# Kernel tuning notes

Hardware: AMD Instinct MI355X
Metric: run time of the kernel (lower is better)

Reference implementation:

```python
import jax, jax.numpy as jnp
import numpy as np

N_NODES = 50000
N_EDGES = 800000
D = 64
NUM_GRAPHS = 64


def setup_inputs() -> dict:
    key = jax.random.key(0)
    ks = jax.random.split(key, 8)
    node_features = jax.random.normal(ks[0], (N_NODES, D), dtype=jnp.float32)
    edge_index = jax.random.randint(ks[1], (2, N_EDGES), 0, N_NODES, dtype=jnp.int32)
    edge_weight = jax.random.uniform(ks[2], (N_EDGES,), dtype=jnp.float32)
    batch = jnp.sort(jax.random.randint(ks[3], (N_NODES,), 0, NUM_GRAPHS, dtype=jnp.int32))
    scale = 1.0 / np.sqrt(D)
    W1 = jax.random.normal(ks[4], (D, D), dtype=jnp.float32) * scale
    b1 = jnp.zeros((D,), dtype=jnp.float32)
    W2 = jax.random.normal(ks[5], (D, D), dtype=jnp.float32) * scale
    b2 = jnp.zeros((D,), dtype=jnp.float32)
    return {"node_features": node_features, "edge_index": edge_index,
            "edge_weight": edge_weight, "batch": batch,
            "W1": W1, "b1": b1, "W2": W2, "b2": b2}


def gcn_conv(x, row, col, ew, W, b, n_nodes):
    # PyG GCNConv: add self-loops (weight 1), symmetric normalization,
    # x' = norm-weighted scatter of (x @ W) over edges, plus bias.
    loop = jnp.arange(n_nodes, dtype=row.dtype)
    r = jnp.concatenate([row, loop])
    c = jnp.concatenate([col, loop])
    w = jnp.concatenate([ew, jnp.ones((n_nodes,), dtype=ew.dtype)])
    deg = jax.ops.segment_sum(w, c, num_segments=n_nodes)  # [N]
    dis = jnp.where(deg > 0, jax.lax.rsqrt(deg), 0.0)
    norm = dis[r] * w * dis[c]                             # [E+N]
    xw = x @ W                                             # [N, D_out]
    msg = xw[r] * norm[:, None]                            # gather + scale
    out = jax.ops.segment_sum(msg, c, num_segments=n_nodes)
    return out + b


def reference(node_features, edge_index, edge_weight, batch, W1, b1, W2, b2):
    row, col = edge_index[0], edge_index[1]
    x = node_features.astype(jnp.float32)
    # conv layers (all but final pooling layer) each followed by ReLU
    x = jax.nn.relu(gcn_conv(x, row, col, edge_weight, W1, b1, N_NODES))
    x = jax.nn.relu(gcn_conv(x, row, col, edge_weight, W2, b2, N_NODES))
    # MeanAggregation pooling over graph ids
    sums = jax.ops.segment_sum(x, batch, num_segments=NUM_GRAPHS)       # [G, D]
    cnts = jax.ops.segment_sum(jnp.ones((x.shape[0],), x.dtype), batch,
                               num_segments=NUM_GRAPHS)                 # [G]
    return sums / jnp.maximum(cnts, 1.0)[:, None]
```

## Files before the change

### kernel.cpp

```cpp
#include <hip/hip_runtime.h>
#include <hip/hip_fp16.h>

#define NN 50000
#define NE 800000
#define DD 64
#define NG 64

#define NBKT 196
#define MAXB 5120
#define SRTB 7168
#define P1CH 2048
#define P1NB ((NE + P1CH - 1) / P1CH)

__global__ __launch_bounds__(256) void bin_k(const int* __restrict__ ei,
                                             const float* __restrict__ ew,
                                             int* __restrict__ bucket_cnt,
                                             unsigned int* __restrict__ tmp_pay,
                                             unsigned char* __restrict__ tmp_c8) {
    __shared__ int hist[NBKT];
    __shared__ int basec[NBKT];
    const int t = threadIdx.x;
    const int e0 = blockIdx.x * P1CH;
    for (int i = t; i < NBKT; i += 256) hist[i] = 0;
    __syncthreads();
    int rr[8]; int cc[8]; float wwf[8];
    #pragma unroll
    for (int i = 0; i < 8; ++i) {
        int e = e0 + i * 256 + t;
        if (e < NE) {
            rr[i] = ei[e]; cc[i] = ei[NE + e]; wwf[i] = ew[e];
            atomicAdd(&hist[cc[i] >> 8], 1);
        } else cc[i] = -1;
    }
    __syncthreads();
    for (int i = t; i < NBKT; i += 256)
        basec[i] = (hist[i] > 0) ? (i * MAXB + atomicAdd(&bucket_cnt[i], hist[i])) : 0;
    __syncthreads();
    #pragma unroll
    for (int i = 0; i < 8; ++i) {
        if (cc[i] >= 0) {
            int b = cc[i] >> 8;
            int slot = atomicAdd(&basec[b], 1);
            unsigned int hb = (unsigned int)__half_as_ushort(__float2half(wwf[i]));
            tmp_pay[slot] = (hb << 16) | (unsigned int)rr[i];
            tmp_c8[slot] = (unsigned char)(cc[i] & 255);
        }
    }
}

__global__ __launch_bounds__(256) void build_k(const int* __restrict__ bucket_cnt,
                                               const unsigned int* __restrict__ tmp_pay,
                                               const unsigned char* __restrict__ tmp_c8,
                                               unsigned int* __restrict__ srt,
                                               int2* __restrict__ rowse,
                                               float* __restrict__ dis) {
    __shared__ int hist[256];
    __shared__ int cursor[256];
    __shared__ float degf[256];
    __shared__ int wtot[4];
    const int b = blockIdx.x;
    const int t = threadIdx.x;
    const int cntb = bucket_cnt[b];
    const int tbase = b * MAXB;
    hist[t] = 0; degf[t] = 0.0f;
    __syncthreads();
    for (int i = t; i < cntb; i += 256) atomicAdd(&hist[tmp_c8[tbase + i]], 1);
    __syncthreads();
    const int v = hist[t];
    const int pv = (v + 7) & ~7;
    int pre = pv;
    #pragma unroll
    for (int off = 1; off < 64; off <<= 1) {
        int u = __shfl_up(pre, off);
        if ((t & 63) >= off) pre += u;
    }
    if ((t & 63) == 63) wtot[t >> 6] = pre;
    __syncthreads();
    int woff = 0;
    for (int i = 0; i < (t >> 6); ++i) woff += wtot[i];
    const int start = b * SRTB + woff + pre - pv;
    cursor[t] = start;
    __syncthreads();
    for (int i = t; i < cntb; i += 256) {
        unsigned int u = tmp_pay[tbase + i];
        int c8 = tmp_c8[tbase + i];
        int slot = atomicAdd(&cursor[c8], 1);
        srt[slot] = u;
        float w = __half2float(__ushort_as_half((unsigned short)(u >> 16)));
        atomicAdd(&degf[c8], w);
    }
    __syncthreads();
    for (int i = start + v; i < start + pv; ++i) srt[i] = 0u;
    const int node = b * 256 + t;
    if (node < NN) {
        rowse[node] = make_int2(start, pv);
        dis[node] = rsqrtf(1.0f + degf[t]);
    }
}

template<bool ACT>
__global__ __launch_bounds__(256, 4) void gemm_k(
    const float* __restrict__ X, const float* __restrict__ W,
    const float* __restrict__ bias_prev, const float* __restrict__ dis,
    __half* __restrict__ Ah)
{
    __shared__ float Ws[64][64];
    __shared__ float Xs[64][68];
    const int t = threadIdx.x;
    const int row0 = blockIdx.x * 64;

    #pragma unroll
    for (int s = t; s < 64 * 64; s += 256) ((float*)Ws)[s] = W[s];
    #pragma unroll
    for (int s = t; s < 64 * 64; s += 256) {
        int r = s >> 6, k = s & 63;
        int row = row0 + r;
        if (row >= NN) row = NN - 1;
        float v = X[(size_t)row * DD + k];
        if (ACT) v = fmaxf(v + bias_prev[k], 0.0f);
        Xs[r][k] = v;
    }
    __syncthreads();

    const int tc = t & 15;
    const int tr = t >> 4;
    float4 acc[4];
    #pragma unroll
    for (int i = 0; i < 4; ++i) acc[i] = make_float4(0.f, 0.f, 0.f, 0.f);

    #pragma unroll 2
    for (int kc = 0; kc < 16; ++kc) {
        const int k = kc * 4;
        float4 w0 = *reinterpret_cast<const float4*>(&Ws[k + 0][tc * 4]);
        float4 w1 = *reinterpret_cast<const float4*>(&Ws[k + 1][tc * 4]);
        float4 w2 = *reinterpret_cast<const float4*>(&Ws[k + 2][tc * 4]);
        float4 w3 = *reinterpret_cast<const float4*>(&Ws[k + 3][tc * 4]);
        #pragma unroll
        for (int i = 0; i < 4; ++i) {
            float4 xv = *reinterpret_cast<const float4*>(&Xs[tr * 4 + i][k]);
            acc[i].x += xv.x * w0.x + xv.y * w1.x + xv.z * w2.x + xv.w * w3.x;
            acc[i].y += xv.x * w0.y + xv.y * w1.y + xv.z * w2.y + xv.w * w3.y;
            acc[i].z += xv.x * w0.z + xv.y * w1.z + xv.z * w2.z + xv.w * w3.z;
            acc[i].w += xv.x * w0.w + xv.y * w1.w + xv.z * w2.w + xv.w * w3.w;
        }
    }

    #pragma unroll
    for (int i = 0; i < 4; ++i) {
        int row = row0 + tr * 4 + i;
        if (row >= NN) break;
        float d = dis[row];
        __half2 h0 = __floats2half2_rn(acc[i].x * d, acc[i].y * d);
        __half2 h1 = __floats2half2_rn(acc[i].z * d, acc[i].w * d);
        uint2 st;
        st.x = *reinterpret_cast<unsigned int*>(&h0);
        st.y = *reinterpret_cast<unsigned int*>(&h1);
        *reinterpret_cast<uint2*>(&Ah[(size_t)row * DD + tc * 4]) = st;
    }
}

__global__ __launch_bounds__(256) void gather_k(
    const int2* __restrict__ rowse, const unsigned int* __restrict__ srt,
    const float* __restrict__ dis,
    const __half2* __restrict__ Ah2, float* __restrict__ B)
{
    const int node = blockIdx.x * 4 + (threadIdx.x >> 6);
    const int wl = threadIdx.x & 63;
    const int h = wl >> 5;
    const int l = wl & 31;
    if (node >= NN) return;
    const int2 se = rowse[node];
    float ax0 = 0.f, ay0 = 0.f, ax1 = 0.f, ay1 = 0.f;
    if (h == 0) {
        __half2 s = Ah2[(size_t)node * 32 + l];
        ax0 = __half2float(__low2half(s));
        ay0 = __half2float(__high2half(s));
    }
    const unsigned int* p = srt + se.x + h * 4;
    for (int n = se.y; n > 0; n -= 8, p += 8) {
        uint4 u = *reinterpret_cast<const uint4*>(p);
        __half2 a0 = Ah2[(size_t)(u.x & 0xffffu) * 32 + l];
        __half2 a1 = Ah2[(size_t)(u.y & 0xffffu) * 32 + l];
        __half2 a2 = Ah2[(size_t)(u.z & 0xffffu) * 32 + l];
        __half2 a3 = Ah2[(size_t)(u.w & 0xffffu) * 32 + l];
        float w0 = __half2float(__ushort_as_half((unsigned short)(u.x >> 16)));
        float w1 = __half2float(__ushort_as_half((unsigned short)(u.y >> 16)));
        float w2 = __half2float(__ushort_as_half((unsigned short)(u.z >> 16)));
        float w3 = __half2float(__ushort_as_half((unsigned short)(u.w >> 16)));
        ax0 += w0 * __half2float(__low2half(a0));
        ay0 += w0 * __half2float(__high2half(a0));
        ax1 += w1 * __half2float(__low2half(a1));
        ay1 += w1 * __half2float(__high2half(a1));
        ax0 += w2 * __half2float(__low2half(a2));
        ay0 += w2 * __half2float(__high2half(a2));
        ax1 += w3 * __half2float(__low2half(a3));
        ay1 += w3 * __half2float(__high2half(a3));
    }
    float ax = ax0 + ax1, ay = ay0 + ay1;
    ax += __shfl_xor(ax, 32);
    ay += __shfl_xor(ay, 32);
    if (h == 0) {
        float d = dis[node];
        *reinterpret_cast<float2*>(&B[(size_t)node * DD + 2 * l]) =
            make_float2(d * ax, d * ay);
    }
}

__global__ __launch_bounds__(64) void pool(
    const float* __restrict__ B, const float* __restrict__ b2,
    const int* __restrict__ batch,
    float* __restrict__ sums, float* __restrict__ cnts, int n)
{
    const int lane = threadIdx.x;
    const int start = blockIdx.x * 32;
    const int end = min(start + 32, n);
    const float bb = b2[lane];
    float acc = 0.0f;
    int cn = 0;
    int curg = batch[start];
    for (int i = start; i < end; ++i) {
        int g = batch[i];
        if (g != curg) {
            unsafeAtomicAdd(&sums[curg * DD + lane], acc);
            if (lane == 0) unsafeAtomicAdd(&cnts[curg], (float)cn);
            acc = 0.0f; cn = 0; curg = g;
        }
        acc += fmaxf(B[(size_t)i * DD + lane] + bb, 0.0f);
        cn++;
    }
    if (cn > 0) {
        unsafeAtomicAdd(&sums[curg * DD + lane], acc);
        if (lane == 0) unsafeAtomicAdd(&cnts[curg], (float)cn);
    }
}

__global__ void finalize(const float* __restrict__ sums, const float* __restrict__ cnts,
                         float* __restrict__ out) {
    int i = blockIdx.x * blockDim.x + threadIdx.x;
    if (i < NG * DD) {
        int g = i >> 6;
        out[i] = sums[i] / fmaxf(cnts[g], 1.0f);
    }
}

extern "C" void kernel_launch(void* const* d_in, const int* in_sizes, int n_in,
                              void* d_out, int out_size, void* d_ws, size_t ws_size,
                              hipStream_t stream) {
    const float* x   = (const float*)d_in[0];
    const int*   ei  = (const int*)  d_in[1];
    const float* ew  = (const float*)d_in[2];
    const int*   bat = (const int*)  d_in[3];
    const float* W1  = (const float*)d_in[4];
    const float* b1  = (const float*)d_in[5];
    const float* W2  = (const float*)d_in[6];
    const float* b2  = (const float*)d_in[7];
    float* out = (float*)d_out;

    char* ws = (char*)d_ws;
    size_t off = 0;
    __half* Ah        = (__half*)(ws + off); off += (size_t)NN * DD * 2;
    float*  B         = (float*) (ws + off); off += (size_t)NN * DD * 4;
    unsigned int* srt = (unsigned int*)(ws + off); off += (size_t)NBKT * SRTB * 4;
    unsigned int* tmp_pay = (unsigned int*)(ws + off); off += (size_t)NBKT * MAXB * 4;
    unsigned char* tmp_c8 = (unsigned char*)(ws + off); off += (size_t)NBKT * MAXB;
    int2*   rowse      = (int2*)(ws + off); off += (size_t)NN * 8;
    float*  dis        = (float*)(ws + off); off += (size_t)NN * 4;
    int*    bucket_cnt = (int*)  (ws + off); off += (size_t)NBKT * 4;
    float*  sums       = (float*)(ws + off); off += (size_t)NG * DD * 4;
    float*  cnts       = (float*)(ws + off); off += (size_t)NG * 4;

    (void)hipMemsetAsync(bucket_cnt, 0, (size_t)(NBKT + NG * DD + NG) * 4, stream);

    bin_k<<<P1NB, 256, 0, stream>>>(ei, ew, bucket_cnt, tmp_pay, tmp_c8);
    build_k<<<NBKT, 256, 0, stream>>>(bucket_cnt, tmp_pay, tmp_c8, srt, rowse, dis);

    gemm_k<false><<<(NN + 63) / 64, 256, 0, stream>>>(x, W1, nullptr, dis, Ah);
    gather_k<<<(NN + 3) / 4, 256, 0, stream>>>(rowse, srt, dis, (const __half2*)Ah, B);

    gemm_k<true><<<(NN + 63) / 64, 256, 0, stream>>>(B, W2, b1, dis, Ah);
    gather_k<<<(NN + 3) / 4, 256, 0, stream>>>(rowse, srt, dis, (const __half2*)Ah, B);

    pool<<<(NN + 31) / 32, 64, 0, stream>>>(B, b2, bat, sums, cnts, NN);
    finalize<<<(NG * DD + 255) / 256, 256, 0, stream>>>(sums, cnts, out);
}
```

Baseline: 139.6 us.

## Store aggregated features in fp16 and split CSR build into quarter-buckets

The intermediate aggregation output B is now stored as fp16 instead of fp32, which halves its write traffic in the gather kernels and its read traffic in the second GEMM and in pooling. The build kernel is split four ways per bucket (784 blocks instead of 196), each handling 64 destination nodes, to raise parallelism. Each of the four blocks re-scans the whole bucket and discards three quarters of the entries, so redundant reads are added. fp16 storage of B also adds rounding error and a risk of overflow before the bias and ReLU.

```diff
diff --git a/kernel.cpp b/kernel.cpp
--- a/kernel.cpp
+++ b/kernel.cpp
@@ -8,7 +8,7 @@
 
 #define NBKT 196
 #define MAXB 5120
-#define SRTB 7168
+#define SRTQ 1792
 #define P1CH 2048
 #define P1NB ((NE + P1CH - 1) / P1CH)
 
@@ -54,53 +54,59 @@
                                                unsigned int* __restrict__ srt,
                                                int2* __restrict__ rowse,
                                                float* __restrict__ dis) {
-    __shared__ int hist[256];
-    __shared__ int cursor[256];
-    __shared__ float degf[256];
-    __shared__ int wtot[4];
-    const int b = blockIdx.x;
+    __shared__ int hist[64];
+    __shared__ int cursor[64];
+    __shared__ float degf[64];
+    const int bq = blockIdx.x;
+    const int b = bq >> 2, q = bq & 3;
     const int t = threadIdx.x;
     const int cntb = bucket_cnt[b];
     const int tbase = b * MAXB;
-    hist[t] = 0; degf[t] = 0.0f;
-    __syncthreads();
-    for (int i = t; i < cntb; i += 256) atomicAdd(&hist[tmp_c8[tbase + i]], 1);
-    __syncthreads();
-    const int v = hist[t];
-    const int pv = (v + 7) & ~7;
-    int pre = pv;
-    #pragma unroll
-    for (int off = 1; off < 64; off <<= 1) {
-        int u = __shfl_up(pre, off);
-        if ((t & 63) >= off) pre += u;
-    }
-    if ((t & 63) == 63) wtot[t >> 6] = pre;
-    __syncthreads();
-    int woff = 0;
-    for (int i = 0; i < (t >> 6); ++i) woff += wtot[i];
-    const int start = b * SRTB + woff + pre - pv;
-    cursor[t] = start;
+    if (t < 64) { hist[t] = 0; degf[t] = 0.0f; }
     __syncthreads();
     for (int i = t; i < cntb; i += 256) {
-        unsigned int u = tmp_pay[tbase + i];
         int c8 = tmp_c8[tbase + i];
-        int slot = atomicAdd(&cursor[c8], 1);
-        srt[slot] = u;
-        float w = __half2float(__ushort_as_half((unsigned short)(u >> 16)));
-        atomicAdd(&degf[c8], w);
-    }
-    __syncthreads();
-    for (int i = start + v; i < start + pv; ++i) srt[i] = 0u;
-    const int node = b * 256 + t;
-    if (node < NN) {
-        rowse[node] = make_int2(start, pv);
-        dis[node] = rsqrtf(1.0f + degf[t]);
-    }
-}
-
-template<bool ACT>
+        if ((c8 >> 6) == q) atomicAdd(&hist[c8 & 63], 1);
+    }
+    __syncthreads();
+    int v = 0, pv = 0, excl = 0;
+    if (t < 64) {
+        v = hist[t];
+        pv = (v + 7) & ~7;
+        int pre = pv;
+        #pragma unroll
+        for (int off = 1; off < 64; off <<= 1) {
+            int u = __shfl_up(pre, off);
+            if (t >= off) pre += u;
+        }
+        excl = bq * SRTQ + pre - pv;
+        cursor[t] = excl;
+    }
+    __syncthreads();
+    for (int i = t; i < cntb; i += 256) {
+        int c8 = tmp_c8[tbase + i];
+        if ((c8 >> 6) == q) {
+            unsigned int u = tmp_pay[tbase + i];
+            int slot = atomicAdd(&cursor[c8 & 63], 1);
+            srt[slot] = u;
+            float w = __half2float(__ushort_as_half((unsigned short)(u >> 16)));
+            atomicAdd(&degf[c8 & 63], w);
+        }
+    }
+    __syncthreads();
+    if (t < 64) {
+        for (int i = excl + v; i < excl + pv; ++i) srt[i] = 0u;
+        const int node = b * 256 + q * 64 + t;
+        if (node < NN) {
+            rowse[node] = make_int2(excl, pv);
+            dis[node] = rsqrtf(1.0f + degf[t]);
+        }
+    }
+}
+
+template<bool ACT, typename TIN>
 __global__ __launch_bounds__(256, 4) void gemm_k(
-    const float* __restrict__ X, const float* __restrict__ W,
+    const TIN* __restrict__ X, const float* __restrict__ W,
     const float* __restrict__ bias_prev, const float* __restrict__ dis,
     __half* __restrict__ Ah)
 {
@@ -116,7 +122,7 @@
         int r = s >> 6, k = s & 63;
         int row = row0 + r;
         if (row >= NN) row = NN - 1;
-        float v = X[(size_t)row * DD + k];
+        float v = static_cast<float>(X[(size_t)row * DD + k]);
         if (ACT) v = fmaxf(v + bias_prev[k], 0.0f);
         Xs[r][k] = v;
     }
@@ -162,7 +168,7 @@
 __global__ __launch_bounds__(256) void gather_k(
     const int2* __restrict__ rowse, const unsigned int* __restrict__ srt,
     const float* __restrict__ dis,
-    const __half2* __restrict__ Ah2, float* __restrict__ B)
+    const __half2* __restrict__ Ah2, __half* __restrict__ Bh)
 {
     const int node = blockIdx.x * 4 + (threadIdx.x >> 6);
     const int wl = threadIdx.x & 63;
@@ -201,13 +207,13 @@
     ay += __shfl_xor(ay, 32);
     if (h == 0) {
         float d = dis[node];
-        *reinterpret_cast<float2*>(&B[(size_t)node * DD + 2 * l]) =
-            make_float2(d * ax, d * ay);
+        __half2 hv = __floats2half2_rn(d * ax, d * ay);
+        *reinterpret_cast<__half2*>(&Bh[(size_t)node * DD + 2 * l]) = hv;
     }
 }
 
 __global__ __launch_bounds__(64) void pool(
-    const float* __restrict__ B, const float* __restrict__ b2,
+    const __half* __restrict__ Bh, const float* __restrict__ b2,
     const int* __restrict__ batch,
     float* __restrict__ sums, float* __restrict__ cnts, int n)
 {
@@ -225,7 +231,7 @@
             if (lane == 0) unsafeAtomicAdd(&cnts[curg], (float)cn);
             acc = 0.0f; cn = 0; curg = g;
         }
-        acc += fmaxf(B[(size_t)i * DD + lane] + bb, 0.0f);
+        acc += fmaxf(__half2float(Bh[(size_t)i * DD + lane]) + bb, 0.0f);
         cn++;
     }
     if (cn > 0) {
@@ -259,8 +265,8 @@
     char* ws = (char*)d_ws;
     size_t off = 0;
     __half* Ah        = (__half*)(ws + off); off += (size_t)NN * DD * 2;
-    float*  B         = (float*) (ws + off); off += (size_t)NN * DD * 4;
-    unsigned int* srt = (unsigned int*)(ws + off); off += (size_t)NBKT * SRTB * 4;
+    __half* Bh        = (__half*)(ws + off); off += (size_t)NN * DD * 2;
+    unsigned int* srt = (unsigned int*)(ws + off); off += (size_t)NBKT * 4 * SRTQ * 4;
     unsigned int* tmp_pay = (unsigned int*)(ws + off); off += (size_t)NBKT * MAXB * 4;
     unsigned char* tmp_c8 = (unsigned char*)(ws + off); off += (size_t)NBKT * MAXB;
     int2*   rowse      = (int2*)(ws + off); off += (size_t)NN * 8;
@@ -272,14 +278,14 @@
     (void)hipMemsetAsync(bucket_cnt, 0, (size_t)(NBKT + NG * DD + NG) * 4, stream);
 
     bin_k<<<P1NB, 256, 0, stream>>>(ei, ew, bucket_cnt, tmp_pay, tmp_c8);
-    build_k<<<NBKT, 256, 0, stream>>>(bucket_cnt, tmp_pay, tmp_c8, srt, rowse, dis);
-
-    gemm_k<false><<<(NN + 63) / 64, 256, 0, stream>>>(x, W1, nullptr, dis, Ah);
-    gather_k<<<(NN + 3) / 4, 256, 0, stream>>>(rowse, srt, dis, (const __half2*)Ah, B);
-
-    gemm_k<true><<<(NN + 63) / 64, 256, 0, stream>>>(B, W2, b1, dis, Ah);
-    gather_k<<<(NN + 3) / 4, 256, 0, stream>>>(rowse, srt, dis, (const __half2*)Ah, B);
-
-    pool<<<(NN + 31) / 32, 64, 0, stream>>>(B, b2, bat, sums, cnts, NN);
+    build_k<<<NBKT * 4, 256, 0, stream>>>(bucket_cnt, tmp_pay, tmp_c8, srt, rowse, dis);
+
+    gemm_k<false, float><<<(NN + 63) / 64, 256, 0, stream>>>(x, W1, nullptr, dis, Ah);
+    gather_k<<<(NN + 3) / 4, 256, 0, stream>>>(rowse, srt, dis, (const __half2*)Ah, Bh);
+
+    gemm_k<true, __half><<<(NN + 63) / 64, 256, 0, stream>>>(Bh, W2, b1, dis, Ah);
+    gather_k<<<(NN + 3) / 4, 256, 0, stream>>>(rowse, srt, dis, (const __half2*)Ah, Bh);
+
+    pool<<<(NN + 31) / 32, 64, 0, stream>>>(Bh, b2, bat, sums, cnts, NN);
     finalize<<<(NG * DD + 255) / 256, 256, 0, stream>>>(sums, cnts, out);
 }
```

Measured after the change: 144.4 us. 1.03x slower.

## Gather 16-byte feature chunks per lane with 8 edges in flight per wave

Applied to the files above, without the earlier changes.

The aggregation kernel now has each lane load a full 16-byte slice (8 halves) of a neighbor row instead of a 4-byte half2, so 8 lanes cover a 64-wide row and a wave processes 8 edge groups of 2 edges in parallel. This is meant to raise bytes per load instruction and memory-level parallelism on the random row gathers. Each node's edge list is now padded to a multiple of 16 (with a larger sorted-edge buffer) to match, and partial sums are reduced with three cross-lane shuffles per accumulator. The cost is more padding work on low-degree nodes, extra shuffle traffic and higher register use.

```diff
diff --git a/kernel.cpp b/kernel.cpp
--- a/kernel.cpp
+++ b/kernel.cpp
@@ -8,7 +8,7 @@
 
 #define NBKT 196
 #define MAXB 5120
-#define SRTB 7168
+#define SRTB 9216
 #define P1CH 2048
 #define P1NB ((NE + P1CH - 1) / P1CH)
 
@@ -67,7 +67,7 @@
     for (int i = t; i < cntb; i += 256) atomicAdd(&hist[tmp_c8[tbase + i]], 1);
     __syncthreads();
     const int v = hist[t];
-    const int pv = (v + 7) & ~7;
+    const int pv = (v + 15) & ~15;
     int pre = pv;
     #pragma unroll
     for (int off = 1; off < 64; off <<= 1) {
@@ -162,47 +162,54 @@
 __global__ __launch_bounds__(256) void gather_k(
     const int2* __restrict__ rowse, const unsigned int* __restrict__ srt,
     const float* __restrict__ dis,
-    const __half2* __restrict__ Ah2, float* __restrict__ B)
+    const uint4* __restrict__ Ah8,
+    float* __restrict__ B)
 {
     const int node = blockIdx.x * 4 + (threadIdx.x >> 6);
     const int wl = threadIdx.x & 63;
-    const int h = wl >> 5;
-    const int l = wl & 31;
+    const int o = wl >> 3;
+    const int l = wl & 7;
     if (node >= NN) return;
     const int2 se = rowse[node];
-    float ax0 = 0.f, ay0 = 0.f, ax1 = 0.f, ay1 = 0.f;
-    if (h == 0) {
-        __half2 s = Ah2[(size_t)node * 32 + l];
-        ax0 = __half2float(__low2half(s));
-        ay0 = __half2float(__high2half(s));
-    }
-    const unsigned int* p = srt + se.x + h * 4;
-    for (int n = se.y; n > 0; n -= 8, p += 8) {
-        uint4 u = *reinterpret_cast<const uint4*>(p);
-        __half2 a0 = Ah2[(size_t)(u.x & 0xffffu) * 32 + l];
-        __half2 a1 = Ah2[(size_t)(u.y & 0xffffu) * 32 + l];
-        __half2 a2 = Ah2[(size_t)(u.z & 0xffffu) * 32 + l];
-        __half2 a3 = Ah2[(size_t)(u.w & 0xffffu) * 32 + l];
+    float acc[8] = {0.f, 0.f, 0.f, 0.f, 0.f, 0.f, 0.f, 0.f};
+    if (o == 0) {
+        uint4 s = Ah8[(size_t)node * 8 + l];
+        const __half2* sh = reinterpret_cast<const __half2*>(&s);
+        #pragma unroll
+        for (int j = 0; j < 4; ++j) {
+            acc[2 * j]     = __half2float(__low2half(sh[j]));
+            acc[2 * j + 1] = __half2float(__high2half(sh[j]));
+        }
+    }
+    const unsigned int* p = srt + se.x + 2 * o;
+    for (int n = se.y; n > 0; n -= 16, p += 16) {
+        uint2 u = *reinterpret_cast<const uint2*>(p);
+        uint4 r0 = Ah8[(size_t)(u.x & 0xffffu) * 8 + l];
+        uint4 r1 = Ah8[(size_t)(u.y & 0xffffu) * 8 + l];
         float w0 = __half2float(__ushort_as_half((unsigned short)(u.x >> 16)));
         float w1 = __half2float(__ushort_as_half((unsigned short)(u.y >> 16)));
-        float w2 = __half2float(__ushort_as_half((unsigned short)(u.z >> 16)));
-        float w3 = __half2float(__ushort_as_half((unsigned short)(u.w >> 16)));
-        ax0 += w0 * __half2float(__low2half(a0));
-        ay0 += w0 * __half2float(__high2half(a0));
-        ax1 += w1 * __half2float(__low2half(a1));
-        ay1 += w1 * __half2float(__high2half(a1));
-        ax0 += w2 * __half2float(__low2half(a2));
-        ay0 += w2 * __half2float(__high2half(a2));
-        ax1 += w3 * __half2float(__low2half(a3));
-        ay1 += w3 * __half2float(__high2half(a3));
-    }
-    float ax = ax0 + ax1, ay = ay0 + ay1;
-    ax += __shfl_xor(ax, 32);
-    ay += __shfl_xor(ay, 32);
-    if (h == 0) {
+        const __half2* h0 = reinterpret_cast<const __half2*>(&r0);
+        const __half2* h1 = reinterpret_cast<const __half2*>(&r1);
+        #pragma unroll
+        for (int j = 0; j < 4; ++j) {
+            acc[2 * j]     += w0 * __half2float(__low2half(h0[j]));
+            acc[2 * j + 1] += w0 * __half2float(__high2half(h0[j]));
+            acc[2 * j]     += w1 * __half2float(__low2half(h1[j]));
+            acc[2 * j + 1] += w1 * __half2float(__high2half(h1[j]));
+        }
+    }
+    #pragma unroll
+    for (int j = 0; j < 8; ++j) {
+        acc[j] += __shfl_xor(acc[j], 8);
+        acc[j] += __shfl_xor(acc[j], 16);
+        acc[j] += __shfl_xor(acc[j], 32);
+    }
+    if (o == 0) {
         float d = dis[node];
-        *reinterpret_cast<float2*>(&B[(size_t)node * DD + 2 * l]) =
-            make_float2(d * ax, d * ay);
+        float4 v0 = make_float4(d * acc[0], d * acc[1], d * acc[2], d * acc[3]);
+        float4 v1 = make_float4(d * acc[4], d * acc[5], d * acc[6], d * acc[7]);
+        *reinterpret_cast<float4*>(&B[(size_t)node * DD + 8 * l]) = v0;
+        *reinterpret_cast<float4*>(&B[(size_t)node * DD + 8 * l + 4]) = v1;
     }
 }
 
@@ -275,10 +282,10 @@
     build_k<<<NBKT, 256, 0, stream>>>(bucket_cnt, tmp_pay, tmp_c8, srt, rowse, dis);
 
     gemm_k<false><<<(NN + 63) / 64, 256, 0, stream>>>(x, W1, nullptr, dis, Ah);
-    gather_k<<<(NN + 3) / 4, 256, 0, stream>>>(rowse, srt, dis, (const __half2*)Ah, B);
+    gather_k<<<(NN + 3) / 4, 256, 0, stream>>>(rowse, srt, dis, (const uint4*)Ah, B);
 
     gemm_k<true><<<(NN + 63) / 64, 256, 0, stream>>>(B, W2, b1, dis, Ah);
-    gather_k<<<(NN + 3) / 4, 256, 0, stream>>>(rowse, srt, dis, (const __half2*)Ah, B);
+    gather_k<<<(NN + 3) / 4, 256, 0, stream>>>(rowse, srt, dis, (const uint4*)Ah, B);
 
     pool<<<(NN + 31) / 32, 64, 0, stream>>>(B, b2, bat, sums, cnts, NN);
     finalize<<<(NG * DD + 255) / 256, 256, 0, stream>>>(sums, cnts, out);
```

Result: no change. 137.1 us (-1.8%).
